# Performance work log

Measured on AMD Instinct MI355X. Metric: run time of the kernel, lower is better.

Reference implementation:

```python
import jax, jax.numpy as jnp
import numpy as np
from jax import lax

D = 256          # embed_dims
NLP = 2          # NumLinePoints
B, H, W = 4, 64, 64
NQ = H * W       # 4096
NK = 4096
BN_EPS = 0.001


def setup_inputs() -> dict:
    key = jax.random.key(0)
    ks = jax.random.split(key, 16)
    inp = {
        "query": jax.random.normal(ks[0], (B, D, H, W), jnp.float32),
        "v": jax.random.normal(ks[1], (B, NK, D), jnp.float32),
        "query_pos": jax.random.normal(ks[2], (B, NQ, D), jnp.float32),
        "key_pos": jax.random.normal(ks[3], (B, NK, D), jnp.float32),
        "other_W": jax.random.uniform(ks[4], (B, NK), jnp.float32),
        # params (torch Linear convention: weight [out, in], y = x @ W.T + b)
        "w_vs": jax.random.normal(ks[5], (D, D), jnp.float32) * (1.0 / np.sqrt(D)),
        "mlp_w1": jax.random.normal(ks[6], (D, 2 * D), jnp.float32) * (1.0 / np.sqrt(2 * D)),
        "mlp_b1": jnp.zeros((D,), jnp.float32),
        "mlp_w2": jax.random.normal(ks[7], (D, D), jnp.float32) * (1.0 / np.sqrt(D)),
        "mlp_b2": jnp.zeros((D,), jnp.float32),
        "conv1_w": jax.random.normal(ks[8], (D, D, 3, 3), jnp.float32) * (1.0 / np.sqrt(9 * D)),
        "bn_gamma": jnp.ones((D,), jnp.float32),
        "bn_beta": jnp.zeros((D,), jnp.float32),
        "bn_mean": jnp.zeros((D,), jnp.float32),
        "bn_var": jnp.ones((D,), jnp.float32),
        "conv2_w": jax.random.normal(ks[9], (D, D, 1, 1), jnp.float32) * (1.0 / np.sqrt(D)),
        "conv2_b": jnp.zeros((D,), jnp.float32),
    }
    return inp


def _forward(query, v, query_pos, key_pos, other_W,
             w_vs, mlp_w1, mlp_b1, mlp_w2, mlp_b2,
             conv1_w, bn_gamma, bn_beta, bn_mean, bn_var,
             conv2_w, conv2_b):
    # v projection (no bias)
    v = jnp.einsum('bkd,ed->bke', v, w_vs)
    # ref_point_head: repeat query_pos along feature dim, then 2-layer MLP
    qp = jnp.concatenate([query_pos] * NLP, axis=-1)          # [B,NQ,2D]
    qp = jax.nn.relu(jnp.einsum('bqd,hd->bqh', qp, mlp_w1) + mlp_b1)
    qp = jnp.einsum('bqh,eh->bqe', qp, mlp_w2) + mlp_b2       # [B,NQ,D]
    # L2 normalize
    qn = qp / jnp.linalg.norm(qp, axis=-1, keepdims=True)
    kn = key_pos / jnp.linalg.norm(key_pos, axis=-1, keepdims=True)
    # similarity + ReLU + elementwise mask
    rel = jax.nn.relu(jnp.einsum('bqd,bkd->bqk', qn, kn))     # [B,NQ,NK]
    rel = rel * other_W[:, None, :]
    out = jnp.einsum('bqk,bkd->bqd', rel, v)                  # [B,NQ,D]
    # reshape to feature map [B,D,H,W]
    out = out.transpose(0, 2, 1).reshape(query.shape)
    # fuse: conv3x3 (no bias) + BN (eval) + SiLU, then conv1x1 (+bias)
    x = lax.conv_general_dilated(out, conv1_w, (1, 1), 'SAME',
                                 dimension_numbers=('NCHW', 'OIHW', 'NCHW'))
    inv = bn_gamma / jnp.sqrt(bn_var + BN_EPS)
    x = x * inv[None, :, None, None] + (bn_beta - bn_mean * inv)[None, :, None, None]
    x = x * jax.nn.sigmoid(x)  # SiLU
    x = lax.conv_general_dilated(x, conv2_w, (1, 1), 'SAME',
                                 dimension_numbers=('NCHW', 'OIHW', 'NCHW'))
    x = x + conv2_b[None, :, None, None]
    return query + x


def reference(query, v, query_pos, key_pos, other_W,
              w_vs, mlp_w1, mlp_b1, mlp_w2, mlp_b2,
              conv1_w, bn_gamma, bn_beta, bn_mean, bn_var,
              conv2_w, conv2_b):
    return _forward(query, v, query_pos, key_pos, other_W,
                    w_vs, mlp_w1, mlp_b1, mlp_w2, mlp_b2,
                    conv1_w, bn_gamma, bn_beta, bn_mean, bn_var,
                    conv2_w, conv2_b)
```

## Files before the change

### kernel.cpp

```cpp
#include <hip/hip_runtime.h>
#include <math.h>

constexpr int kB  = 4;
constexpr int kD  = 256;
constexpr int kNQ = 4096;
constexpr int kNK = 4096;
constexpr int kHW = 4096;

typedef __bf16 bf16x8 __attribute__((ext_vector_type(8)));
typedef float  f32x16 __attribute__((ext_vector_type(16)));

__device__ __forceinline__ unsigned short f2bf(float x) {
    unsigned int u = __builtin_bit_cast(unsigned int, x);
    u = (u + 0x7fffu + ((u >> 16) & 1u)) >> 16;
    return (unsigned short)u;
}

__global__ __launch_bounds__(256) void k_prep(
    const float* __restrict__ v_in, const float* __restrict__ ow, ushort* __restrict__ v_bf,
    const float* __restrict__ qpos, ushort* __restrict__ qpos_bf,
    const float* __restrict__ kpos, ushort* __restrict__ kn_bf,
    const float* __restrict__ conv1_w, ushort* __restrict__ w9p,
    const float* __restrict__ w_vs, ushort* __restrict__ wvs_bf,
    const float* __restrict__ mlp_w2, ushort* __restrict__ w2_bf,
    const float* __restrict__ conv2_w, ushort* __restrict__ c2_bf,
    const float* __restrict__ mlp_w1, ushort* __restrict__ w1e_bf)
{
    const int bid = blockIdx.x, t = threadIdx.x;
    if (bid < 4096) {
        const int i = bid * 256 + t;
        float4 v = ((const float4*)v_in)[i];
        const float wsc = ow[i >> 6];
        ushort4 o;
        o.x = f2bf(v.x * wsc); o.y = f2bf(v.y * wsc);
        o.z = f2bf(v.z * wsc); o.w = f2bf(v.w * wsc);
        ((ushort4*)v_bf)[i] = o;
    } else if (bid < 8192) {
        const int i = (bid - 4096) * 256 + t;
        float4 v = ((const float4*)qpos)[i];
        ushort4 o;
        o.x = f2bf(v.x); o.y = f2bf(v.y); o.z = f2bf(v.z); o.w = f2bf(v.w);
        ((ushort4*)qpos_bf)[i] = o;
    } else if (bid < 12288) {
        const int row  = (bid - 8192) * 4 + (t >> 6);
        const int lane = t & 63;
        float4 v = ((const float4*)(kpos + (size_t)row * 256))[lane];
        float ss = v.x * v.x + v.y * v.y + v.z * v.z + v.w * v.w;
        #pragma unroll
        for (int off = 32; off; off >>= 1) ss += __shfl_xor(ss, off, 64);
        const float rn = 1.0f / sqrtf(ss);
        ushort4 o;
        o.x = f2bf(v.x * rn); o.y = f2bf(v.y * rn);
        o.z = f2bf(v.z * rn); o.w = f2bf(v.w * rn);
        ((ushort4*)(kn_bf + (size_t)row * 256))[lane] = o;
    } else if (bid < 14592) {
        const int idx = bid - 12288;
        const int s = idx >> 8, co = idx & 255, ci = t;
        const int oidx = ((s * 8 + (co >> 5)) * 16 + (ci >> 4)) * 512
                       + ((ci >> 3) & 1) * 256 + (co & 31) * 8 + (ci & 7);
        w9p[oidx] = f2bf(conv1_w[((size_t)co * 256 + ci) * 9 + s]);
    } else if (bid < 14784) {
        const float* src = (bid < 14656) ? w_vs : (bid < 14720) ? mlp_w2 : conv2_w;
        ushort* dst = (bid < 14656) ? wvs_bf : (bid < 14720) ? w2_bf : c2_bf;
        const int i = ((bid - 14592) & 63) * 256 + t;
        float4 v = ((const float4*)src)[i];
        ushort4 o;
        o.x = f2bf(v.x); o.y = f2bf(v.y); o.z = f2bf(v.z); o.w = f2bf(v.w);
        ((ushort4*)dst)[i] = o;
    } else {
        const int h = bid - 14784;
        w1e_bf[h * 256 + t] = f2bf(mlp_w1[h * 512 + t] + mlp_w1[h * 512 + 256 + t]);
    }
}

template<int EPI, int RELU>
__global__ __launch_bounds__(512, 1) void k_gemm_mfma(
    const ushort* __restrict__ A, const ushort* __restrict__ W,
    const float* __restrict__ bias, void* __restrict__ outp)
{
    __shared__ __align__(16) char lds[131072];
    const int t = threadIdx.x, w = t >> 6, l = t & 63, lr = l & 31, lh = l >> 5;
    const int wm = w >> 2, wn = w & 3;
    const int m0 = (blockIdx.x >> 1) * 128;
    const int n0 = (blockIdx.x & 1) * 128;
    const char* Ab = (const char*)A + (size_t)m0 * 512;
    const char* Wb = (const char*)W + (size_t)n0 * 512;
    #pragma unroll
    for (int i = 0; i < 8; ++i) {
        const int p = i * 512 + t;
        const int R = p >> 5, sl = p & 31;
        const int so = R * 512 + ((sl ^ (R & 31)) << 4);
        __builtin_amdgcn_global_load_lds(
            (const __attribute__((address_space(1))) unsigned*)(Ab + so),
            (__attribute__((address_space(3))) unsigned*)(lds + p * 16), 16, 0, 0);
        __builtin_amdgcn_global_load_lds(
            (const __attribute__((address_space(1))) unsigned*)(Wb + so),
            (__attribute__((address_space(3))) unsigned*)(lds + 65536 + p * 16), 16, 0, 0);
    }
    __syncthreads();
    const char* Abuf = lds;
    const char* Wbuf = lds + 65536;
    const int ar0 = wm * 64 + lr, ar1 = ar0 + 32;
    const int wrr = wn * 32 + lr;
    f32x16 c0{}, c1{};
    #pragma unroll
    for (int ks = 0; ks < 16; ++ks) {
        const int j = 2 * ks + lh;
        bf16x8 a0 = *(const bf16x8*)(Abuf + ar0 * 512 + ((j ^ lr) << 4));
        bf16x8 a1 = *(const bf16x8*)(Abuf + ar1 * 512 + ((j ^ lr) << 4));
        bf16x8 wf = *(const bf16x8*)(Wbuf + wrr * 512 + ((j ^ lr) << 4));
        c0 = __builtin_amdgcn_mfma_f32_32x32x16_bf16(a0, wf, c0, 0, 0, 0);
        c1 = __builtin_amdgcn_mfma_f32_32x32x16_bf16(a1, wf, c1, 0, 0, 0);
    }
    const int n = n0 + wn * 32 + lr;
    float bb = bias ? bias[n] : 0.f;
    if constexpr (EPI == 2) {
        __syncthreads();
        ushort (*tr)[136] = (ushort(*)[136])lds;
        #pragma unroll
        for (int r = 0; r < 16; ++r) {
            const int ml = wm * 64 + (r & 3) + 8 * (r >> 2) + 4 * lh;
            float v0 = c0[r], v1 = c1[r];
            if (RELU) { v0 = fmaxf(v0, 0.f); v1 = fmaxf(v1, 0.f); }
            tr[wn * 32 + lr][ml]      = f2bf(v0);
            tr[wn * 32 + lr][ml + 32] = f2bf(v1);
        }
        __syncthreads();
        ushort* out = (ushort*)outp;
        const int b = m0 >> 12, mm = m0 & 4095;
        const int row = t >> 2, seg = t & 3;
        uint4 u0 = *(uint4*)&tr[row][seg * 32];
        uint4 u1 = *(uint4*)&tr[row][seg * 32 + 8];
        uint4 u2 = *(uint4*)&tr[row][seg * 32 + 16];
        uint4 u3 = *(uint4*)&tr[row][seg * 32 + 24];
        ushort* ob = out + ((size_t)(b * 128 + (mm >> 5) + seg) * 256 + n0 + row) * 32;
        *(uint4*)ob        = u0; *(uint4*)(ob + 8)  = u1;
        *(uint4*)(ob + 16) = u2; *(uint4*)(ob + 24) = u3;
    } else {
        #pragma unroll
        for (int r = 0; r < 16; ++r) {
            const int m = m0 + wm * 64 + (r & 3) + 8 * (r >> 2) + 4 * lh;
            float v0 = c0[r] + bb, v1 = c1[r] + bb;
            if (RELU) { v0 = fmaxf(v0, 0.f); v1 = fmaxf(v1, 0.f); }
            if constexpr (EPI == 0) {
                float* out = (float*)outp;
                out[(size_t)m * 256 + n]      = v0;
                out[(size_t)(m + 32) * 256 + n] = v1;
            } else {
                ushort* out = (ushort*)outp;
                out[(size_t)m * 256 + n]      = f2bf(v0);
                out[(size_t)(m + 32) * 256 + n] = f2bf(v1);
            }
        }
    }
}

__global__ __launch_bounds__(256) void k_l2norm_bf16(const float* __restrict__ in,
                                                     ushort* __restrict__ out) {
    const int row  = blockIdx.x * 4 + (threadIdx.x >> 6);
    const int lane = threadIdx.x & 63;
    float4 v = ((const float4*)(in + (size_t)row * 256))[lane];
    float ss = v.x * v.x + v.y * v.y + v.z * v.z + v.w * v.w;
    #pragma unroll
    for (int off = 32; off; off >>= 1) ss += __shfl_xor(ss, off, 64);
    const float rn = 1.0f / sqrtf(ss);
    ushort4 o;
    o.x = f2bf(v.x * rn); o.y = f2bf(v.y * rn);
    o.z = f2bf(v.z * rn); o.w = f2bf(v.w * rn);
    ((ushort4*)(out + (size_t)row * 256))[lane] = o;
}

__global__ __launch_bounds__(512, 2) void k_attn_mfma(
    const ushort* __restrict__ qn, const ushort* __restrict__ kn,
    const ushort* __restrict__ vpT, ushort* __restrict__ X)
{
    __shared__ __align__(16) char lds[147456];
    const int t = threadIdx.x, w = t >> 6, l = t & 63, lr = l & 31, lh = l >> 5;
    const int dh = w >> 2, qg = (w >> 1) & 1, kh = w & 1;
    const int bid0 = blockIdx.x;
    const int L = (bid0 & 7) * 32 + (bid0 >> 3);
    const int b = L >> 6, qt = L & 63;
    const int q0 = qt << 6;
    union U4 { unsigned u[4]; bf16x8 v; };

    int koff[4], voff[4];
    #pragma unroll
    for (int i = 0; i < 4; ++i) {
        const int p = i * 512 + t;
        {
            const int R = p >> 5, sl = p & 31;
            koff[i] = R * 512 + ((sl ^ (R & 31)) << 4);
        }
        {
            const int sub = p >> 10, q = p & 1023;
            const int R = q >> 4, ch = (q & 15) ^ (R & 15);
            voff[i] = sub * 16384 + ((ch >> 2) * 64 + R) * 64 + ((ch & 3) << 4);
        }
    }
    const char* kgb = (const char*)(kn + (size_t)b * 4096 * 256);
    const char* vgb = (const char*)vpT + (size_t)b * 128 * 16384;

    #define STAGE_K(bb, tc) do { \
        const char* ks_ = kgb + (size_t)(tc) * 32768; \
        char* kd_ = lds + (bb) * 32768; \
        _Pragma("unroll") \
        for (int i_ = 0; i_ < 4; ++i_) \
            __builtin_amdgcn_global_load_lds( \
                (const __attribute__((address_space(1))) unsigned*)(ks_ + koff[i_]), \
                (__attribute__((address_space(3))) unsigned*)(kd_ + (i_ * 512 + w * 64) * 16), 16, 0, 0); \
        } while (0)
    #define STAGE_V(bb, tc) do { \
        const char* vs_ = vgb + (size_t)(tc) * 32768; \
        char* vd_ = lds + 65536 + (bb) * 32768; \
        _Pragma("unroll") \
        for (int i_ = 0; i_ < 4; ++i_) \
            __builtin_amdgcn_global_load_lds( \
                (const __attribute__((address_space(1))) unsigned*)(vs_ + voff[i_]), \
                (__attribute__((address_space(3))) unsigned*)(vd_ + (i_ * 512 + w * 64) * 16), 16, 0, 0); \
        } while (0)

    const ushort* qrow = qn + ((size_t)b * 4096 + q0 + qg * 32 + lr) * 256 + lh * 8;
    bf16x8 qf[16];
    #pragma unroll
    for (int ks = 0; ks < 16; ++ks) qf[ks] = *(const bf16x8*)(qrow + ks * 16);

    f32x16 oa0{}, oa1{}, oa2{}, oa3{};
    bf16x8 pf0{}, pf1{};

    STAGE_K(0, 0);
    __syncthreads();
    for (int tt = 0; tt <= 64; ++tt) {
        if (tt < 64) {
            if (tt + 1 < 64) STAGE_K((tt + 1) & 1, tt + 1);
            STAGE_V(tt & 1, tt);
        }
        if (tt > 0) {
            const char* vb = lds + 65536 + ((tt - 1) & 1) * 32768 + kh * 16384;
            bf16x8 qp0, qp1;
            if (dh == 0) { qp0 = pf0; qp1 = pf1; }
            else {
                const unsigned* pr = (const unsigned*)(lds + 131072
                                   + ((tt - 1) & 1) * 8192 + (qg * 2 + kh) * 2048);
                U4 a0, a1;
                #pragma unroll
                for (int wd = 0; wd < 4; ++wd) {
                    a0.u[wd] = pr[wd * 64 + l];
                    a1.u[wd] = pr[(4 + wd) * 64 + l];
                }
                qp0 = a0.v; qp1 = a1.v;
            }
            #define PVD(OA, DB) { \
                const int R_  = (((DB) & 1)) * 32 + lr; \
                const int sg_ = dh * 2 + ((DB) >> 1); \
                bf16x8 v0_ = *(const bf16x8*)(vb + R_ * 256 + ((((sg_ << 2) + lh)     ^ (lr & 15)) << 4)); \
                bf16x8 v1_ = *(const bf16x8*)(vb + R_ * 256 + ((((sg_ << 2) + 2 + lh) ^ (lr & 15)) << 4)); \
                OA = __builtin_amdgcn_mfma_f32_32x32x16_bf16(v0_, qp0, OA, 0, 0, 0); \
                OA = __builtin_amdgcn_mfma_f32_32x32x16_bf16(v1_, qp1, OA, 0, 0, 0); }
            PVD(oa0, 0) PVD(oa1, 1) PVD(oa2, 2) PVD(oa3, 3)
            #undef PVD
        }
        if (dh == 0 && tt < 64) {
            const char* kb = lds + (tt & 1) * 32768 + kh * 16384;
            f32x16 s0{}, s1{}, s2{}, s3{};
            #pragma unroll
            for (int ks = 0; ks < 16; ks += 4) {
                bf16x8 k0 = *(const bf16x8*)(kb + lr * 512 + (((2 * ks     + lh) ^ lr) << 4));
                bf16x8 k1 = *(const bf16x8*)(kb + lr * 512 + (((2 * ks + 2 + lh) ^ lr) << 4));
                bf16x8 k2 = *(const bf16x8*)(kb + lr * 512 + (((2 * ks + 4 + lh) ^ lr) << 4));
                bf16x8 k3 = *(const bf16x8*)(kb + lr * 512 + (((2 * ks + 6 + lh) ^ lr) << 4));
                s0 = __builtin_amdgcn_mfma_f32_32x32x16_bf16(k0, qf[ks],     s0, 0, 0, 0);
                s1 = __builtin_amdgcn_mfma_f32_32x32x16_bf16(k1, qf[ks + 1], s1, 0, 0, 0);
                s2 = __builtin_amdgcn_mfma_f32_32x32x16_bf16(k2, qf[ks + 2], s2, 0, 0, 0);
                s3 = __builtin_amdgcn_mfma_f32_32x32x16_bf16(k3, qf[ks + 3], s3, 0, 0, 0);
            }
            f32x16 s = (s0 + s1) + (s2 + s3);
            #define PKR(A, B) ((unsigned)f2bf(fmaxf((A), 0.f)) | ((unsigned)f2bf(fmaxf((B), 0.f)) << 16))
            unsigned p01 = PKR(s[0],  s[1]),  p23 = PKR(s[2],  s[3]);
            unsigned p45 = PKR(s[4],  s[5]),  p67 = PKR(s[6],  s[7]);
            unsigned p89 = PKR(s[8],  s[9]),  pAB = PKR(s[10], s[11]);
            unsigned pCD = PKR(s[12], s[13]), pEF = PKR(s[14], s[15]);
            #undef PKR
            unsigned e1a = lh ? p01 : p45,  e2a = lh ? p23 : p67;
            unsigned e1b = lh ? p89 : pCD,  e2b = lh ? pAB : pEF;
            unsigned f1a = (unsigned)__shfl_xor((int)e1a, 32, 64);
            unsigned f2a = (unsigned)__shfl_xor((int)e2a, 32, 64);
            unsigned f1b = (unsigned)__shfl_xor((int)e1b, 32, 64);
            unsigned f2b = (unsigned)__shfl_xor((int)e2b, 32, 64);
            U4 a0, a1;
            a0.u[0] = lh ? f1a : p01;  a0.u[1] = lh ? f2a : p23;
            a0.u[2] = lh ? p45 : f1a;  a0.u[3] = lh ? p67 : f2a;
            a1.u[0] = lh ? f1b : p89;  a1.u[1] = lh ? f2b : pAB;
            a1.u[2] = lh ? pCD : f1b;  a1.u[3] = lh ? pEF : f2b;
            pf0 = a0.v; pf1 = a1.v;
            unsigned* pw = (unsigned*)(lds + 131072 + (tt & 1) * 8192 + (qg * 2 + kh) * 2048);
            #pragma unroll
            for (int wd = 0; wd < 4; ++wd) {
                pw[wd * 64 + l]       = a0.u[wd];
                pw[(4 + wd) * 64 + l] = a1.u[wd];
            }
        }
        if (tt < 64) __syncthreads();
    }
    #undef STAGE_K
    #undef STAGE_V
    float* red = (float*)lds;
    const int rowbase = ((qg * 2 + dh) * 32 + lr) * 132;
    if (kh == 1) {
        #define REDW(OA, DB) _Pragma("unroll") \
            for (int r = 0; r < 16; r += 2) { \
                const int d_ = (DB) * 32 + (r & 3) + 8 * (r >> 2) + 4 * lh; \
                *(float2*)&red[rowbase + d_] = make_float2((OA)[r], (OA)[r + 1]); }
        REDW(oa0, 0) REDW(oa1, 1) REDW(oa2, 2) REDW(oa3, 3)
        #undef REDW
    }
    __syncthreads();
    if (kh == 0) {
        ushort* Xb = X + ((size_t)b * 4096 + q0 + qg * 32 + lr) * 256 + dh * 128;
        #define OUTD(OA, DB) _Pragma("unroll") \
            for (int r = 0; r < 16; r += 2) { \
                const int d_ = (DB) * 32 + (r & 3) + 8 * (r >> 2) + 4 * lh; \
                float2 p = *(float2*)&red[rowbase + d_]; \
                ushort2 u_; u_.x = f2bf((OA)[r] + p.x); u_.y = f2bf((OA)[r + 1] + p.y); \
                *(ushort2*)(Xb + d_) = u_; }
        OUTD(oa0, 0) OUTD(oa1, 1) OUTD(oa2, 2) OUTD(oa3, 3)
        #undef OUTD
    }
}

__global__ __launch_bounds__(256, 2) void k_conv3_mfma(
    const ushort* __restrict__ X, const ushort* __restrict__ w9p,
    const float* __restrict__ bn_g, const float* __restrict__ bn_b,
    const float* __restrict__ bn_m, const float* __restrict__ bn_v,
    ushort* __restrict__ Y)
{
    __shared__ __align__(16) char smem[67584];
    float* bnv = (float*)(smem + 65536);
    const int t = threadIdx.x, w = t >> 6, l = t & 63, lr = l & 31, lh = l >> 5;
    {
        float inv = bn_g[t] * rsqrtf(bn_v[t] + 1e-3f);
        bnv[t]       = inv;
        bnv[256 + t] = bn_b[t] - bn_m[t] * inv;
    }
    const int bid = blockIdx.x;
    const int b = bid >> 7, ct = (bid >> 5) & 3, pt = bid & 31;
    const int co0 = ct * 64, p0 = pt * 128;
    const int wc = w >> 1, wp = w & 1;
    const int h0 = pt * 2 + wp;
    const int cb = ct * 2 + wc;
    const char* Xbytes = (const char*)(X + (size_t)b * 4096 * 256);
    const bf16x8 bz = {};
    f32x16 o0{}, o1{};

    #define CSTAGE(bufb, st_) do { \
        const char* src_ = Xbytes + (ptrdiff_t)(p0 + 64 * ((st_) >> 1) - 64) * 512 \
                         + ((st_) & 1) * 256; \
        char* dst_ = smem + (bufb) * 32768; \
        _Pragma("unroll") \
        for (int i_ = 0; i_ < 8; ++i_) { \
            const int di_ = i_ * 256 + t; \
            const int R_ = di_ >> 4, sl_ = di_ & 15; \
            __builtin_amdgcn_global_load_lds( \
                (const __attribute__((address_space(1))) unsigned*)(src_ + (ptrdiff_t)R_ * 512 + ((sl_ ^ (R_ & 15)) << 4)), \
                (__attribute__((address_space(3))) unsigned*)(dst_ + di_ * 16), 16, 0, 0); \
        } } while (0)

    CSTAGE(0, 0);
    __syncthreads();
    for (int st = 0; st < 6; ++st) {
        if (st < 5) CSTAGE((st + 1) & 1, st + 1);
        if (st < 5) asm volatile("s_waitcnt vmcnt(8)" ::: "memory");
        else        asm volatile("s_waitcnt vmcnt(0)" ::: "memory");
        __builtin_amdgcn_s_barrier();
        const char* xb = smem + (st & 1) * 32768;
        const int dyi = st >> 1, cih = st & 1;
        const int hh = h0 + dyi - 1;
        if (hh >= 0 && hh <= 63) {
            __builtin_amdgcn_s_setprio(1);
            #pragma unroll
            for (int dxi = 0; dxi < 3; ++dxi) {
                const int dx = dxi - 1;
                const int s = dyi * 3 + dxi;
                const bool mA = (dxi == 0) && (lr == 0);
                const bool mB = (dxi == 2) && (lr == 31);
                const int R0 = mA ? 0 : (wp * 64 + lr + dx);
                const int R1 = mB ? 0 : (wp * 64 + lr + dx + 32);
                const ushort* wb = w9p + ((size_t)(s * 8 + cb) * 16 + cih * 8) * 512 + l * 8;
                #pragma unroll
                for (int k8 = 0; k8 < 8; ++k8) {
                    bf16x8 af = *(const bf16x8*)(wb + k8 * 512);
                    bf16x8 b0 = *(const bf16x8*)(xb + R0 * 256 + (((k8 * 2 + lh) ^ (R0 & 15)) << 4));
                    bf16x8 b1 = *(const bf16x8*)(xb + R1 * 256 + (((k8 * 2 + lh) ^ (R1 & 15)) << 4));
                    if (mA) b0 = bz;
                    if (mB) b1 = bz;
                    o0 = __builtin_amdgcn_mfma_f32_32x32x16_bf16(af, b0, o0, 0, 0, 0);
                    o1 = __builtin_amdgcn_mfma_f32_32x32x16_bf16(af, b1, o1, 0, 0, 0);
                }
            }
            __builtin_amdgcn_s_setprio(0);
        }
        __builtin_amdgcn_s_barrier();
    }
    #undef CSTAGE
    ushort (*tr)[72] = (ushort(*)[72])smem;
    #pragma unroll
    for (int r = 0; r < 16; ++r) {
        const int co_l = wc * 32 + (r & 3) + 8 * (r >> 2) + 4 * lh;
        const int co = co0 + co_l;
        const float inv = bnv[co], add = bnv[256 + co];
        float x0 = o0[r] * inv + add;
        float x1 = o1[r] * inv + add;
        x0 = x0 / (1.f + expf(-x0));
        x1 = x1 / (1.f + expf(-x1));
        tr[wp * 64 + lr][co_l]      = f2bf(x0);
        tr[wp * 64 + 32 + lr][co_l] = f2bf(x1);
    }
    __syncthreads();
    const int pp = t >> 1, half = t & 1;
    uint4 u0 = *(uint4*)&tr[pp][half * 32];
    uint4 u1 = *(uint4*)&tr[pp][half * 32 + 8];
    uint4 u2 = *(uint4*)&tr[pp][half * 32 + 16];
    uint4 u3 = *(uint4*)&tr[pp][half * 32 + 24];
    ushort* yb = Y + ((size_t)b * 4096 + p0 + pp) * 256 + co0 + half * 32;
    *(uint4*)yb        = u0; *(uint4*)(yb + 8)  = u1;
    *(uint4*)(yb + 16) = u2; *(uint4*)(yb + 24) = u3;
}

__global__ __launch_bounds__(512, 1) void k_conv1x1_mfma(
    const ushort* __restrict__ Y, const ushort* __restrict__ W2,
    const float* __restrict__ bias2, const float* __restrict__ query,
    float* __restrict__ out)
{
    __shared__ __align__(16) char lds[131072];
    const int t = threadIdx.x, w = t >> 6, l = t & 63, lr = l & 31, lh = l >> 5;
    const int wc = w >> 2, wp = w & 3;
    const int bid = blockIdx.x;
    const int b = bid >> 6, pt = (bid >> 1) & 31, ct = bid & 1;
    const int p0 = pt * 128, co0 = ct * 128;
    const char* Yb = (const char*)Y + ((size_t)b * 4096 + p0) * 512;
    const char* Wb = (const char*)W2 + (size_t)co0 * 512;
    #pragma unroll
    for (int i = 0; i < 8; ++i) {
        const int p = i * 512 + t;
        const int R = p >> 5, sl = p & 31;
        const int so = R * 512 + ((sl ^ (R & 31)) << 4);
        __builtin_amdgcn_global_load_lds(
            (const __attribute__((address_space(1))) unsigned*)(Yb + so),
            (__attribute__((address_space(3))) unsigned*)(lds + p * 16), 16, 0, 0);
        __builtin_amdgcn_global_load_lds(
            (const __attribute__((address_space(1))) unsigned*)(Wb + so),
            (__attribute__((address_space(3))) unsigned*)(lds + 65536 + p * 16), 16, 0, 0);
    }
    __syncthreads();
    const char* Ybuf = lds;
    const char* Wbuf = lds + 65536;
    const int cr0 = wc * 64 + lr, cr1 = cr0 + 32;
    const int yr  = wp * 32 + lr;
    f32x16 o0{}, o1{};
    #pragma unroll
    for (int ks = 0; ks < 16; ++ks) {
        const int j = 2 * ks + lh;
        bf16x8 w0 = *(const bf16x8*)(Wbuf + cr0 * 512 + ((j ^ lr) << 4));
        bf16x8 w1 = *(const bf16x8*)(Wbuf + cr1 * 512 + ((j ^ lr) << 4));
        bf16x8 yf = *(const bf16x8*)(Ybuf + yr  * 512 + ((j ^ lr) << 4));
        o0 = __builtin_amdgcn_mfma_f32_32x32x16_bf16(w0, yf, o0, 0, 0, 0);
        o1 = __builtin_amdgcn_mfma_f32_32x32x16_bf16(w1, yf, o1, 0, 0, 0);
    }
    const int p = p0 + wp * 32 + lr;
    #pragma unroll
    for (int r = 0; r < 16; ++r) {
        const int crow = (r & 3) + 8 * (r >> 2) + 4 * lh;
        const int coA = co0 + wc * 64 + crow;
        const int coB = coA + 32;
        const size_t baseA = ((size_t)b * 256 + coA) * 4096 + p;
        const size_t baseB = ((size_t)b * 256 + coB) * 4096 + p;
        out[baseA] = o0[r] + bias2[coA] + query[baseA];
        out[baseB] = o1[r] + bias2[coB] + query[baseB];
    }
}

extern "C" void kernel_launch(void* const* d_in, const int* in_sizes, int n_in,
                              void* d_out, int out_size, void* d_ws, size_t ws_size,
                              hipStream_t stream) {
    const float* query   = (const float*)d_in[0];
    const float* v_in    = (const float*)d_in[1];
    const float* qpos    = (const float*)d_in[2];
    const float* kpos    = (const float*)d_in[3];
    const float* otherW  = (const float*)d_in[4];
    const float* w_vs    = (const float*)d_in[5];
    const float* mlp_w1  = (const float*)d_in[6];
    const float* mlp_b1  = (const float*)d_in[7];
    const float* mlp_w2  = (const float*)d_in[8];
    const float* mlp_b2  = (const float*)d_in[9];
    const float* conv1_w = (const float*)d_in[10];
    const float* bn_g    = (const float*)d_in[11];
    const float* bn_b    = (const float*)d_in[12];
    const float* bn_m    = (const float*)d_in[13];
    const float* bn_v    = (const float*)d_in[14];
    const float* conv2_w = (const float*)d_in[15];
    const float* conv2_b = (const float*)d_in[16];
    float* out = (float*)d_out;
    char* base = (char*)d_ws;

    constexpr size_t MB = 1u << 20;
    ushort* v_bf    = (ushort*)(base);
    ushort* qpos_bf = (ushort*)(base + 8 * MB);
    float*  qp_f32  = (float*) (base);
    ushort* qhid_bf = (ushort*)(base + 16 * MB);
    ushort* X_bf    = (ushort*)(base + 16 * MB);
    ushort* qn_bf   = (ushort*)(base + 24 * MB);
    ushort* Y_bf    = (ushort*)(base + 24 * MB);
    ushort* kn_bf   = (ushort*)(base + 32 * MB);
    ushort* vT_bf   = (ushort*)(base + 40 * MB);
    ushort* wvs_bf  = (ushort*)(base + 48 * MB);
    ushort* w1e_bf  = (ushort*)(base + 48 * MB + 128 * 1024);
    ushort* w2_bf   = (ushort*)(base + 48 * MB + 256 * 1024);
    ushort* c2_bf   = (ushort*)(base + 48 * MB + 384 * 1024);
    ushort* w9p_bf  = (ushort*)(base + 48 * MB + 512 * 1024);

    k_prep<<<15040, 256, 0, stream>>>(v_in, otherW, v_bf, qpos, qpos_bf,
                                      kpos, kn_bf, conv1_w, w9p_bf,
                                      w_vs, wvs_bf, mlp_w2, w2_bf,
                                      conv2_w, c2_bf, mlp_w1, w1e_bf);
    k_gemm_mfma<2, 0><<<256, 512, 0, stream>>>(v_bf, wvs_bf, nullptr, vT_bf);
    k_gemm_mfma<1, 1><<<256, 512, 0, stream>>>(qpos_bf, w1e_bf, mlp_b1, qhid_bf);
    k_gemm_mfma<0, 0><<<256, 512, 0, stream>>>(qhid_bf, w2_bf, mlp_b2, qp_f32);
    k_l2norm_bf16<<<4096, 256, 0, stream>>>(qp_f32, qn_bf);
    k_attn_mfma<<<256, 512, 0, stream>>>(qn_bf, kn_bf, vT_bf, X_bf);
    k_conv3_mfma<<<512, 256, 0, stream>>>(X_bf, w9p_bf, bn_g, bn_b, bn_m, bn_v, Y_bf);
    k_conv1x1_mfma<<<256, 512, 0, stream>>>(Y_bf, c2_bf, conv2_b, query, out);
}
```

Measured before the change: 183.7 us.

## Fuse query L2-normalization into attention kernel and raise MFMA wave priority

Removes the separate L2-norm kernel. The attention kernel now loads the unnormalized fp32 query projection, converts it to bf16 and computes the row norm in registers. The 1/norm scale is applied after ReLU to the similarity scores, which works because the scale is positive. This saves a kernel launch and one round trip of the normalized query through memory. It also wraps the MFMA sections in s_setprio to favour the matrix work during scheduling. The cost is that scores are now computed from unnormalized bf16 queries, which changes rounding slightly.

```diff
diff --git a/kernel.cpp b/kernel.cpp
--- a/kernel.cpp
+++ b/kernel.cpp
@@ -155,23 +155,8 @@
     }
 }
 
-__global__ __launch_bounds__(256) void k_l2norm_bf16(const float* __restrict__ in,
-                                                     ushort* __restrict__ out) {
-    const int row  = blockIdx.x * 4 + (threadIdx.x >> 6);
-    const int lane = threadIdx.x & 63;
-    float4 v = ((const float4*)(in + (size_t)row * 256))[lane];
-    float ss = v.x * v.x + v.y * v.y + v.z * v.z + v.w * v.w;
-    #pragma unroll
-    for (int off = 32; off; off >>= 1) ss += __shfl_xor(ss, off, 64);
-    const float rn = 1.0f / sqrtf(ss);
-    ushort4 o;
-    o.x = f2bf(v.x * rn); o.y = f2bf(v.y * rn);
-    o.z = f2bf(v.z * rn); o.w = f2bf(v.w * rn);
-    ((ushort4*)(out + (size_t)row * 256))[lane] = o;
-}
-
 __global__ __launch_bounds__(512, 2) void k_attn_mfma(
-    const ushort* __restrict__ qn, const ushort* __restrict__ kn,
+    const float* __restrict__ qpf, const ushort* __restrict__ kn,
     const ushort* __restrict__ vpT, ushort* __restrict__ X)
 {
     __shared__ __align__(16) char lds[147456];
@@ -219,10 +204,27 @@
                 (__attribute__((address_space(3))) unsigned*)(vd_ + (i_ * 512 + w * 64) * 16), 16, 0, 0); \
         } while (0)
 
-    const ushort* qrow = qn + ((size_t)b * 4096 + q0 + qg * 32 + lr) * 256 + lh * 8;
     bf16x8 qf[16];
-    #pragma unroll
-    for (int ks = 0; ks < 16; ++ks) qf[ks] = *(const bf16x8*)(qrow + ks * 16);
+    float rn = 0.f;
+    if (dh == 0) {
+        const float* qrow = qpf + ((size_t)b * 4096 + q0 + qg * 32 + lr) * 256 + lh * 8;
+        float ss = 0.f;
+        #pragma unroll
+        for (int ks = 0; ks < 16; ++ks) {
+            float4 a = *(const float4*)(qrow + ks * 16);
+            float4 c = *(const float4*)(qrow + ks * 16 + 4);
+            ss += a.x * a.x + a.y * a.y + a.z * a.z + a.w * a.w
+                + c.x * c.x + c.y * c.y + c.z * c.z + c.w * c.w;
+            U4 q8a;
+            q8a.u[0] = (unsigned)f2bf(a.x) | ((unsigned)f2bf(a.y) << 16);
+            q8a.u[1] = (unsigned)f2bf(a.z) | ((unsigned)f2bf(a.w) << 16);
+            q8a.u[2] = (unsigned)f2bf(c.x) | ((unsigned)f2bf(c.y) << 16);
+            q8a.u[3] = (unsigned)f2bf(c.z) | ((unsigned)f2bf(c.w) << 16);
+            qf[ks] = q8a.v;
+        }
+        ss += __shfl_xor(ss, 32, 64);
+        rn = rsqrtf(ss);
+    }
 
     f32x16 oa0{}, oa1{}, oa2{}, oa3{};
     bf16x8 pf0{}, pf1{};
@@ -249,6 +251,7 @@
                 }
                 qp0 = a0.v; qp1 = a1.v;
             }
+            __builtin_amdgcn_s_setprio(1);
             #define PVD(OA, DB) { \
                 const int R_  = (((DB) & 1)) * 32 + lr; \
                 const int sg_ = dh * 2 + ((DB) >> 1); \
@@ -258,10 +261,12 @@
                 OA = __builtin_amdgcn_mfma_f32_32x32x16_bf16(v1_, qp1, OA, 0, 0, 0); }
             PVD(oa0, 0) PVD(oa1, 1) PVD(oa2, 2) PVD(oa3, 3)
             #undef PVD
+            __builtin_amdgcn_s_setprio(0);
         }
         if (dh == 0 && tt < 64) {
             const char* kb = lds + (tt & 1) * 32768 + kh * 16384;
             f32x16 s0{}, s1{}, s2{}, s3{};
+            __builtin_amdgcn_s_setprio(1);
             #pragma unroll
             for (int ks = 0; ks < 16; ks += 4) {
                 bf16x8 k0 = *(const bf16x8*)(kb + lr * 512 + (((2 * ks     + lh) ^ lr) << 4));
@@ -273,8 +278,9 @@
                 s2 = __builtin_amdgcn_mfma_f32_32x32x16_bf16(k2, qf[ks + 2], s2, 0, 0, 0);
                 s3 = __builtin_amdgcn_mfma_f32_32x32x16_bf16(k3, qf[ks + 3], s3, 0, 0, 0);
             }
+            __builtin_amdgcn_s_setprio(0);
             f32x16 s = (s0 + s1) + (s2 + s3);
-            #define PKR(A, B) ((unsigned)f2bf(fmaxf((A), 0.f)) | ((unsigned)f2bf(fmaxf((B), 0.f)) << 16))
+            #define PKR(A, B) ((unsigned)f2bf(fmaxf((A), 0.f) * rn) | ((unsigned)f2bf(fmaxf((B), 0.f) * rn) << 16))
             unsigned p01 = PKR(s[0],  s[1]),  p23 = PKR(s[2],  s[3]);
             unsigned p45 = PKR(s[4],  s[5]),  p67 = PKR(s[6],  s[7]);
             unsigned p89 = PKR(s[8],  s[9]),  pAB = PKR(s[10], s[11]);
@@ -507,7 +513,6 @@
     float*  qp_f32  = (float*) (base);
     ushort* qhid_bf = (ushort*)(base + 16 * MB);
     ushort* X_bf    = (ushort*)(base + 16 * MB);
-    ushort* qn_bf   = (ushort*)(base + 24 * MB);
     ushort* Y_bf    = (ushort*)(base + 24 * MB);
     ushort* kn_bf   = (ushort*)(base + 32 * MB);
     ushort* vT_bf   = (ushort*)(base + 40 * MB);
@@ -524,8 +529,7 @@
     k_gemm_mfma<2, 0><<<256, 512, 0, stream>>>(v_bf, wvs_bf, nullptr, vT_bf);
     k_gemm_mfma<1, 1><<<256, 512, 0, stream>>>(qpos_bf, w1e_bf, mlp_b1, qhid_bf);
     k_gemm_mfma<0, 0><<<256, 512, 0, stream>>>(qhid_bf, w2_bf, mlp_b2, qp_f32);
-    k_l2norm_bf16<<<4096, 256, 0, stream>>>(qp_f32, qn_bf);
-    k_attn_mfma<<<256, 512, 0, stream>>>(qn_bf, kn_bf, vT_bf, X_bf);
+    k_attn_mfma<<<256, 512, 0, stream>>>(qp_f32, kn_bf, vT_bf, X_bf);
     k_conv3_mfma<<<512, 256, 0, stream>>>(X_bf, w9p_bf, bn_g, bn_b, bn_m, bn_v, Y_bf);
     k_conv1x1_mfma<<<256, 512, 0, stream>>>(Y_bf, c2_bf, conv2_b, query, out);
 }
```

Measured after the change: 180.4 us. No clear change (-1.8%).
